# Performance work log

Measured on AMD Instinct MI355X. Metric: run time of the kernel, lower is better.

## Reference

```python
import jax, jax.numpy as jnp
import numpy as np

B, T, D, H = 8, 4096, 1024, 1024


def log_g(x):
    # log of g(x) = relu(x)+0.5 for x>=0, sigmoid(x) for x<0 (continuous at 0)
    return jnp.where(x >= 0, jnp.log(jax.nn.relu(x) + 0.5), -jax.nn.softplus(-x))


def setup_inputs() -> dict:
    key = jax.random.key(0)
    k0, k1, k2, k3, k4, k5 = jax.random.split(key, 6)
    s = 1.0 / np.sqrt(D)
    return {
        "x": jax.random.normal(k0, (B, T, D), jnp.float32),
        "h_0": jax.random.normal(k1, (B, H), jnp.float32),
        "Wz": jax.random.uniform(k2, (H, D), jnp.float32, -s, s),
        "bz": jax.random.uniform(k3, (H,), jnp.float32, -s, s),
        "Wh": jax.random.uniform(k4, (H, D), jnp.float32, -s, s),
        "bh": jax.random.uniform(k5, (H,), jnp.float32, -s, s),
    }


def reference(x, h_0, Wz, bz, Wh, bh):
    # gate pre-activation k: (B,T,H)
    k = jnp.einsum("btd,hd->bth", x, Wz) + bz
    log_z = -jax.nn.softplus(-k)        # log sigmoid(k)
    log_coeffs = -jax.nn.softplus(k)    # log (1 - sigmoid(k))
    log_h_0 = log_g(h_0)[:, None, :]    # (B,1,H)
    log_tilde_h = log_g(jnp.einsum("btd,hd->bth", x, Wh) + bh)
    log_values = jnp.concatenate([log_h_0, log_z + log_tilde_h], axis=1)  # (B,T+1,H)
    # parallel scan in log space
    a_star = jnp.pad(jnp.cumsum(log_coeffs, axis=1), ((0, 0), (1, 0), (0, 0)))
    log_h = a_star + jax.lax.cumlogsumexp(log_values - a_star, axis=1)
    h = jnp.exp(log_h)                  # (B,T+1,H)
    return h[:, -T:, :]
```

## Files before the change

kernel.cpp:

```cpp
#include <hip/hip_runtime.h>
#include <hip/hip_bf16.h>

#define Bb 8
#define Tt 4096
#define Dd 1024
#define Hh 1024
#define Mm (Bb * Tt)
#define NCHUNK 32
#define CLEN 128

typedef float f32x4 __attribute__((ext_vector_type(4)));
typedef short bf16x8 __attribute__((ext_vector_type(8)));

__device__ __forceinline__ unsigned f2bfu(float x) {
  unsigned u = __float_as_uint(x);
  return (u + 0x7fffu + ((u >> 16) & 1u)) >> 16;
}
__device__ __forceinline__ float bflo(unsigned u) { return __uint_as_float(u << 16); }
__device__ __forceinline__ float bfhi(unsigned u) { return __uint_as_float(u & 0xffff0000u); }

__global__ void cvt_kernel(const float* __restrict__ src, unsigned short* __restrict__ dst,
                           int n4) {
  int i = blockIdx.x * blockDim.x + threadIdx.x;
  int stride = gridDim.x * blockDim.x;
  for (; i < n4; i += stride) {
    float4 v = reinterpret_cast<const float4*>(src)[i];
    ushort4 o;
    o.x = (unsigned short)f2bfu(v.x);
    o.y = (unsigned short)f2bfu(v.y);
    o.z = (unsigned short)f2bfu(v.z);
    o.w = (unsigned short)f2bfu(v.w);
    reinterpret_cast<ushort4*>(dst)[i] = o;
  }
}

__device__ __forceinline__ void async16(const unsigned short* g, unsigned short* l) {
  __builtin_amdgcn_global_load_lds(
      (const __attribute__((address_space(1))) unsigned int*)g,
      (__attribute__((address_space(3))) unsigned int*)l, 16, 0, 0);
}

#define SHFL_COMPOSE(A, Q, MASK, HIBIT)                                   \
  {                                                                       \
    const float pA_ = __shfl_xor(A, MASK);                                \
    const float pQ_ = __shfl_xor(Q, MASK);                                \
    const float Alo_ = (HIBIT) ? pA_ : A;                                 \
    const float Qlo_ = (HIBIT) ? pQ_ : Q;                                 \
    const float Ahi_ = (HIBIT) ? A : pA_;                                 \
    const float Qhi_ = (HIBIT) ? Q : pQ_;                                 \
    A = Alo_ * Ahi_;                                                      \
    Q = fmaf(Ahi_, Qlo_, Qhi_);                                           \
  }

__global__ void __launch_bounds__(512, 4) gemm_kernel(
    const unsigned short* __restrict__ xb,
    const unsigned short* __restrict__ wzb,
    const unsigned short* __restrict__ whb,
    const float* __restrict__ bz,
    const float* __restrict__ bh,
    unsigned int* __restrict__ P,
    float* __restrict__ Pp, float* __restrict__ Qq) {
  __shared__ unsigned short lds[36864];
  const int tid = threadIdx.x;
  const int wid = tid >> 6;
  const int wm = wid >> 2;
  const int wn = wid & 3;
  const int l = tid & 63, ln = l & 15, l4 = l >> 4;

  const int id = blockIdx.x;
  const int sw = (id & 7) * 256 + (id >> 3);
  const int mb = sw >> 3, nb = sw & 7;
  const int m0 = mb * 128, h0 = nb * 128;

  const int r0 = tid >> 2;
  const int chunk = ((tid & 3) - r0) & 3;
  const unsigned short* agp = xb + (size_t)(m0 + r0) * Dd + chunk * 8;
  const int sub16 = r0 >> 4;
  const int hrow0 = h0 + ((sub16 >> 1) << 4) + (r0 & 15);
  const unsigned short* bgp =
      ((sub16 & 1) ? whb : wzb) + (size_t)hrow0 * Dd + chunk * 8;
  const int ta = tid * 8;

  auto stage = [&](int buf) {
    unsigned short* d = &lds[buf * 12288];
    async16(agp, d + ta);
    async16(bgp, d + 4096 + ta);
    async16(bgp + (size_t)64 * Dd, d + 8192 + ta);
    agp += 32;
    bgp += 32;
  };

  int oA[4], oB[4];
#pragma unroll
  for (int mf = 0; mf < 4; ++mf) {
    const int row = wm * 64 + mf * 16 + ln;
    const int sl = (l4 + row) & 3;
    oA[mf] = row * 32 + sl * 8;
  }
#pragma unroll
  for (int nf = 0; nf < 4; ++nf) {
    const int row = wn * 64 + nf * 16 + ln;
    const int sl = (l4 + row) & 3;
    oB[nf] = 4096 + row * 32 + sl * 8;
  }

  f32x4 acc[4][4];
#pragma unroll
  for (int i = 0; i < 4; ++i)
#pragma unroll
    for (int j = 0; j < 4; ++j) acc[i][j] = f32x4{0.f, 0.f, 0.f, 0.f};

  stage(0);
  stage(1);

  int cur = 0, nxt = 2;
#pragma unroll 1
  for (int s = 0; s < 32; ++s) {
    asm volatile("s_waitcnt vmcnt(3)" ::: "memory");
    __builtin_amdgcn_s_barrier();
    const unsigned short* bp = &lds[cur * 12288];
    bf16x8 af[4], bf[4];
    af[0] = *(const bf16x8*)(bp + oA[0]);
    af[1] = *(const bf16x8*)(bp + oA[1]);
    af[2] = *(const bf16x8*)(bp + oA[2]);
    af[3] = *(const bf16x8*)(bp + oA[3]);
    bf[0] = *(const bf16x8*)(bp + oB[0]);
    bf[1] = *(const bf16x8*)(bp + oB[1]);
    bf[2] = *(const bf16x8*)(bp + oB[2]);
    bf[3] = *(const bf16x8*)(bp + oB[3]);
    stage(nxt);
    __builtin_amdgcn_s_setprio(1);
#pragma unroll
    for (int i = 0; i < 4; ++i)
#pragma unroll
      for (int j = 0; j < 4; ++j)
        acc[i][j] =
            __builtin_amdgcn_mfma_f32_16x16x32_bf16(af[i], bf[j], acc[i][j], 0, 0, 0);
    __builtin_amdgcn_s_setprio(0);
    cur = (cur + 1) == 3 ? 0 : cur + 1;
    nxt = (nxt + 1) == 3 ? 0 : nxt + 1;
  }

  asm volatile("s_waitcnt vmcnt(0)" ::: "memory");
  __syncthreads();

  float* sA = (float*)lds;
  float* sQ = (float*)lds + 256;
  const int b_idx = mb >> 5;
  const int ch = mb & 31;

#pragma unroll
  for (int p = 0; p < 2; ++p) {
    const int hcol = h0 + (wn * 2 + p) * 16 + ln;
    const float bzv = bz[hcol];
    const float bhv = bh[hcol];
    float Ar = 1.f, Qr = 0.f;
#pragma unroll
    for (int mf = 0; mf < 4; ++mf) {
      float A4 = 1.f, Q4 = 0.f;
#pragma unroll
      for (int q = 0; q < 4; ++q) {
        const int m = m0 + wm * 64 + mf * 16 + l4 * 4 + q;
        const float kv = acc[mf][2 * p][q] + bzv;
        const float pv = acc[mf][2 * p + 1][q] + bhv;
        const float ek = __expf(kv);
        const float a = 1.f / (1.f + ek);
        const float z = 1.f - a;
        const float g = (pv >= 0.f) ? (pv + 0.5f) : (1.f / (1.f + __expf(-pv)));
        const float c = z * g;
        const unsigned pw = f2bfu(a) | (f2bfu(c) << 16);
        P[(size_t)m * Hh + hcol] = pw;
        const float ar = bflo(pw), cr = bfhi(pw);
        Q4 = fmaf(ar, Q4, cr);
        A4 *= ar;
      }
      SHFL_COMPOSE(A4, Q4, 16, (l4 & 1));
      SHFL_COMPOSE(A4, Q4, 32, ((l4 >> 1) & 1));
      Qr = fmaf(A4, Qr, Q4);
      Ar *= A4;
    }
    if (l4 == 0) {
      sA[wm * 128 + (wn * 2 + p) * 16 + ln] = Ar;
      sQ[wm * 128 + (wn * 2 + p) * 16 + ln] = Qr;
    }
  }
  __syncthreads();
  if (tid < 128) {
    const float A0 = sA[tid], Q0 = sQ[tid];
    const float A1 = sA[128 + tid], Q1 = sQ[128 + tid];
    const int idx = ch * (Bb * Hh) + b_idx * Hh + (h0 + tid);
    Pp[idx] = A0 * A1;
    Qq[idx] = fmaf(A1, Q0, Q1);
  }
}

__global__ void scan_pass2(const float* __restrict__ h0raw,
                           const float* __restrict__ Pp, const float* __restrict__ Qq,
                           float* __restrict__ Hinit) {
  const int bh = blockIdx.x * 256 + threadIdx.x;
  const float x = h0raw[bh];
  float hs = (x >= 0.f) ? (x + 0.5f) : (1.f / (1.f + __expf(-x)));
  for (int ch = 0; ch < NCHUNK; ++ch) {
    const int idx = ch * (Bb * Hh) + bh;
    Hinit[idx] = hs;
    hs = fmaf(Pp[idx], hs, Qq[idx]);
  }
}

__global__ void scan_pass3(const unsigned int* __restrict__ P,
                           const float* __restrict__ Hinit,
                           float* __restrict__ out) {
  const int h = blockIdx.x * 256 + threadIdx.x;
  const int ch = blockIdx.y;
  const int b = blockIdx.z;
  float hs = Hinit[ch * (Bb * Hh) + b * Hh + h];
  const size_t base = ((size_t)(b * Tt + ch * CLEN)) * Hh + h;
  const unsigned int* p = P + base;
  float* o = out + base;
#pragma unroll 8
  for (int i = 0; i < CLEN; ++i) {
    const unsigned u = p[(size_t)i * Hh];
    hs = fmaf(bflo(u), hs, bfhi(u));
    o[(size_t)i * Hh] = hs;
  }
}

extern "C" void kernel_launch(void* const* d_in, const int* in_sizes, int n_in,
                              void* d_out, int out_size, void* d_ws, size_t ws_size,
                              hipStream_t stream) {
  const float* x  = (const float*)d_in[0];
  const float* h0 = (const float*)d_in[1];
  const float* Wz = (const float*)d_in[2];
  const float* bz = (const float*)d_in[3];
  const float* Wh = (const float*)d_in[4];
  const float* bh = (const float*)d_in[5];
  float* out = (float*)d_out;

  char* ws = (char*)d_ws;
  unsigned short* xb  = (unsigned short*)(ws);
  unsigned short* wzb = (unsigned short*)(ws + 67108864);
  unsigned short* whb = (unsigned short*)(ws + 69206016);
  unsigned int*   P   = (unsigned int*)(ws + 71303168);
  float* Pp    = (float*)(ws + 205520896);
  float* Qq    = (float*)(ws + 206569472);
  float* Hinit = (float*)(ws + 207618048);

  cvt_kernel<<<4096, 256, 0, stream>>>(x, xb, Mm * Dd / 4);
  cvt_kernel<<<1024, 256, 0, stream>>>(Wz, wzb, Hh * Dd / 4);
  cvt_kernel<<<1024, 256, 0, stream>>>(Wh, whb, Hh * Dd / 4);

  gemm_kernel<<<2048, 512, 0, stream>>>(xb, wzb, whb, bz, bh, P, Pp, Qq);

  scan_pass2<<<Bb * Hh / 256, 256, 0, stream>>>(h0, Pp, Qq, Hinit);
  dim3 sgrid(Hh / 256, NCHUNK, Bb);
  scan_pass3<<<sgrid, 256, 0, stream>>>(P, Hinit, out);
}
```

Before: 266.0 us.

## Load GEMM weight fragments directly to registers and halve N tile

The GEMM block tile shrinks from 128x128 to 128x64, so each block runs 256 threads in a 2x2 wave grid and the grid doubles to 4096 blocks. Only the x tile is still staged through LDS with async copies. Weight fragments are now loaded straight from global memory into registers, double-buffered across an unrolled pair of steps. This cuts LDS traffic and footprint and is meant to raise occupancy. The cost is that x tiles are re-read twice as often and weight loads become uncoalesced, per-lane global reads.

Result: slower. 392.8 us (+47.7%).

```diff
diff --git a/kernel.cpp b/kernel.cpp
--- a/kernel.cpp
+++ b/kernel.cpp
@@ -52,7 +52,7 @@
     Q = fmaf(Ahi_, Qlo_, Qhi_);                                           \
   }
 
-__global__ void __launch_bounds__(512, 4) gemm_kernel(
+__global__ void __launch_bounds__(256, 3) gemm_kernel(
     const unsigned short* __restrict__ xb,
     const unsigned short* __restrict__ wzb,
     const unsigned short* __restrict__ whb,
@@ -60,49 +60,42 @@
     const float* __restrict__ bh,
     unsigned int* __restrict__ P,
     float* __restrict__ Pp, float* __restrict__ Qq) {
-  __shared__ unsigned short lds[36864];
+  __shared__ unsigned short lds[12288];
   const int tid = threadIdx.x;
   const int wid = tid >> 6;
-  const int wm = wid >> 2;
-  const int wn = wid & 3;
+  const int wm = wid >> 1;
+  const int wn = wid & 1;
   const int l = tid & 63, ln = l & 15, l4 = l >> 4;
 
   const int id = blockIdx.x;
-  const int sw = (id & 7) * 256 + (id >> 3);
-  const int mb = sw >> 3, nb = sw & 7;
-  const int m0 = mb * 128, h0 = nb * 128;
-
-  const int r0 = tid >> 2;
-  const int chunk = ((tid & 3) - r0) & 3;
-  const unsigned short* agp = xb + (size_t)(m0 + r0) * Dd + chunk * 8;
-  const int sub16 = r0 >> 4;
-  const int hrow0 = h0 + ((sub16 >> 1) << 4) + (r0 & 15);
-  const unsigned short* bgp =
-      ((sub16 & 1) ? whb : wzb) + (size_t)hrow0 * Dd + chunk * 8;
+  const int sw = (id & 7) * 512 + (id >> 3);
+  const int mb = sw >> 4, nb = sw & 15;
+  const int m0 = mb * 128;
+  const int h0 = nb * 64;
+
+  const int chunk = ((tid & 3) - (tid >> 3)) & 3;
+  const unsigned short* agp = xb + (size_t)(m0 + (tid >> 2)) * Dd + chunk * 8;
   const int ta = tid * 8;
-
   auto stage = [&](int buf) {
-    unsigned short* d = &lds[buf * 12288];
+    unsigned short* d = &lds[buf * 4096];
     async16(agp, d + ta);
-    async16(bgp, d + 4096 + ta);
-    async16(bgp + (size_t)64 * Dd, d + 8192 + ta);
+    async16(agp + (size_t)64 * Dd, d + 2048 + ta);
     agp += 32;
-    bgp += 32;
   };
 
-  int oA[4], oB[4];
+  int oA[4];
 #pragma unroll
   for (int mf = 0; mf < 4; ++mf) {
     const int row = wm * 64 + mf * 16 + ln;
-    const int sl = (l4 + row) & 3;
+    const int sl = (l4 + (row >> 1)) & 3;
     oA[mf] = row * 32 + sl * 8;
   }
-#pragma unroll
-  for (int nf = 0; nf < 4; ++nf) {
-    const int row = wn * 64 + nf * 16 + ln;
-    const int sl = (l4 + row) & 3;
-    oB[nf] = 4096 + row * 32 + sl * 8;
-  }
+
+  const int hc0 = h0 + wn * 32 + ln;
+  const unsigned short* p0 = wzb + (size_t)hc0 * Dd + l4 * 8;
+  const unsigned short* p1 = whb + (size_t)hc0 * Dd + l4 * 8;
+  const unsigned short* p2 = wzb + (size_t)(hc0 + 16) * Dd + l4 * 8;
+  const unsigned short* p3 = whb + (size_t)(hc0 + 16) * Dd + l4 * 8;
 
   f32x4 acc[4][4];
 #pragma unroll
@@ -110,48 +103,62 @@
 #pragma unroll
     for (int j = 0; j < 4; ++j) acc[i][j] = f32x4{0.f, 0.f, 0.f, 0.f};
 
+  bf16x8 b0[4], b1[4];
+
   stage(0);
+  b0[0] = *(const bf16x8*)p0; p0 += 32;
+  b0[1] = *(const bf16x8*)p1; p1 += 32;
+  b0[2] = *(const bf16x8*)p2; p2 += 32;
+  b0[3] = *(const bf16x8*)p3; p3 += 32;
   stage(1);
 
-  int cur = 0, nxt = 2;
+#define STEP(CUR, BUSE, BNXT)                                             \
+  {                                                                       \
+    asm volatile("s_waitcnt vmcnt(2)" ::: "memory");                      \
+    __builtin_amdgcn_s_barrier();                                         \
+    const unsigned short* bp = &lds[(CUR) * 4096];                        \
+    bf16x8 af[4];                                                         \
+    af[0] = *(const bf16x8*)(bp + oA[0]);                                 \
+    af[1] = *(const bf16x8*)(bp + oA[1]);                                 \
+    af[2] = *(const bf16x8*)(bp + oA[2]);                                 \
+    af[3] = *(const bf16x8*)(bp + oA[3]);                                 \
+    BNXT[0] = *(const bf16x8*)p0; p0 += 32;                               \
+    BNXT[1] = *(const bf16x8*)p1; p1 += 32;                               \
+    BNXT[2] = *(const bf16x8*)p2; p2 += 32;                               \
+    BNXT[3] = *(const bf16x8*)p3; p3 += 32;                               \
+    int st_ = (CUR) + 2; if (st_ >= 3) st_ -= 3;                          \
+    stage(st_);                                                           \
+    __builtin_amdgcn_s_setprio(1);                                        \
+    _Pragma("unroll")                                                     \
+    for (int i_ = 0; i_ < 4; ++i_)                                        \
+      _Pragma("unroll")                                                   \
+      for (int j_ = 0; j_ < 4; ++j_)                                      \
+        acc[i_][j_] = __builtin_amdgcn_mfma_f32_16x16x32_bf16(            \
+            af[i_], BUSE[j_], acc[i_][j_], 0, 0, 0);                      \
+    __builtin_amdgcn_s_setprio(0);                                        \
+  }
+
+  int c0 = 0;
 #pragma unroll 1
-  for (int s = 0; s < 32; ++s) {
-    asm volatile("s_waitcnt vmcnt(3)" ::: "memory");
-    __builtin_amdgcn_s_barrier();
-    const unsigned short* bp = &lds[cur * 12288];
-    bf16x8 af[4], bf[4];
-    af[0] = *(const bf16x8*)(bp + oA[0]);
-    af[1] = *(const bf16x8*)(bp + oA[1]);
-    af[2] = *(const bf16x8*)(bp + oA[2]);
-    af[3] = *(const bf16x8*)(bp + oA[3]);
-    bf[0] = *(const bf16x8*)(bp + oB[0]);
-    bf[1] = *(const bf16x8*)(bp + oB[1]);
-    bf[2] = *(const bf16x8*)(bp + oB[2]);
-    bf[3] = *(const bf16x8*)(bp + oB[3]);
-    stage(nxt);
-    __builtin_amdgcn_s_setprio(1);
-#pragma unroll
-    for (int i = 0; i < 4; ++i)
-#pragma unroll
-      for (int j = 0; j < 4; ++j)
-        acc[i][j] =
-            __builtin_amdgcn_mfma_f32_16x16x32_bf16(af[i], bf[j], acc[i][j], 0, 0, 0);
-    __builtin_amdgcn_s_setprio(0);
-    cur = (cur + 1) == 3 ? 0 : cur + 1;
-    nxt = (nxt + 1) == 3 ? 0 : nxt + 1;
-  }
+  for (int it = 0; it < 16; ++it) {
+    STEP(c0, b0, b1);
+    int c1 = c0 + 1; if (c1 == 3) c1 = 0;
+    STEP(c1, b1, b0);
+    c0 = c1 + 1; if (c0 == 3) c0 = 0;
+  }
+#undef STEP
 
   asm volatile("s_waitcnt vmcnt(0)" ::: "memory");
   __syncthreads();
 
   float* sA = (float*)lds;
-  float* sQ = (float*)lds + 256;
+  float* sQ = (float*)lds + 128;
   const int b_idx = mb >> 5;
   const int ch = mb & 31;
 
 #pragma unroll
   for (int p = 0; p < 2; ++p) {
-    const int hcol = h0 + (wn * 2 + p) * 16 + ln;
+    const int hcol = h0 + wn * 32 + p * 16 + ln;
     const float bzv = bz[hcol];
     const float bhv = bh[hcol];
     float Ar = 1.f, Qr = 0.f;
@@ -180,14 +187,14 @@
       Ar *= A4;
     }
     if (l4 == 0) {
-      sA[wm * 128 + (wn * 2 + p) * 16 + ln] = Ar;
-      sQ[wm * 128 + (wn * 2 + p) * 16 + ln] = Qr;
+      sA[wm * 64 + wn * 32 + p * 16 + ln] = Ar;
+      sQ[wm * 64 + wn * 32 + p * 16 + ln] = Qr;
     }
   }
   __syncthreads();
-  if (tid < 128) {
+  if (tid < 64) {
     const float A0 = sA[tid], Q0 = sQ[tid];
-    const float A1 = sA[128 + tid], Q1 = sQ[128 + tid];
+    const float A1 = sA[64 + tid], Q1 = sQ[64 + tid];
     const int idx = ch * (Bb * Hh) + b_idx * Hh + (h0 + tid);
     Pp[idx] = A0 * A1;
     Qq[idx] = fmaf(A1, Q0, Q1);
@@ -249,7 +256,7 @@
   cvt_kernel<<<1024, 256, 0, stream>>>(Wz, wzb, Hh * Dd / 4);
   cvt_kernel<<<1024, 256, 0, stream>>>(Wh, whb, Hh * Dd / 4);
 
-  gemm_kernel<<<2048, 512, 0, stream>>>(xb, wzb, whb, bz, bh, P, Pp, Qq);
+  gemm_kernel<<<4096, 256, 0, stream>>>(xb, wzb, whb, bz, bh, P, Pp, Qq);
 
   scan_pass2<<<Bb * Hh / 256, 256, 0, stream>>>(h0, Pp, Qq, Hinit);
   dim3 sgrid(Hh / 256, NCHUNK, Bb);
```
